# Kernel optimization log

Hardware: AMD Instinct MI355X
Metric: run time of the kernel (lower is better)

## Reference

```python
import jax, jax.numpy as jnp
import numpy as np

N = 50000   # nodes
E = 400000  # edges
H = 4       # heads
C = 64      # hidden per head
IN = 8
G = 64      # graphs in batch
NEG_SLOPE = 0.2


def setup_inputs() -> dict:
    key = jax.random.key(0)
    ks = jax.random.split(key, 32)
    def w(k, shape, fan_in):
        return jax.random.normal(k, shape, jnp.float32) * (1.0 / np.sqrt(fan_in))
    inp = {}
    inp['x'] = jax.random.normal(ks[0], (N, IN), jnp.float32)
    inp['edge_index'] = jax.random.randint(ks[1], (2, E), 0, N, jnp.int32)
    inp['edge_attr'] = jax.random.normal(ks[2], (E, 1), jnp.float32)
    inp['batch'] = jnp.sort(jax.random.randint(ks[3], (N,), 0, G, jnp.int32))
    # encoder
    inp['enc_w'] = w(ks[4], (IN, H * 16), IN)[:, :64]  # [8,64]
    inp['enc_b'] = jnp.zeros((64,), jnp.float32)
    # gat1: in 64 -> H*C = 256
    inp['g1_wl'] = w(ks[5], (64, H * C), 64)
    inp['g1_bl'] = jnp.zeros((H * C,), jnp.float32)
    inp['g1_wr'] = w(ks[6], (64, H * C), 64)
    inp['g1_we'] = w(ks[7], (1, H * C), 1)
    inp['g1_att'] = w(ks[8], (H, C), C)
    inp['g1_b'] = jnp.zeros((H * C,), jnp.float32)
    # gat2: in 256 -> H*C = 256
    inp['g2_wl'] = w(ks[9], (H * C, H * C), H * C)
    inp['g2_bl'] = jnp.zeros((H * C,), jnp.float32)
    inp['g2_wr'] = w(ks[10], (H * C, H * C), H * C)
    inp['g2_we'] = w(ks[11], (1, H * C), 1)
    inp['g2_att'] = w(ks[12], (H, C), C)
    inp['g2_b'] = jnp.zeros((H * C,), jnp.float32)
    # post MLP: 256 -> 128 -> LN -> ReLU -> 128 -> 64 -> ReLU
    inp['p1_w'] = w(ks[13], (H * C, 128), H * C)
    inp['p1_b'] = jnp.zeros((128,), jnp.float32)
    inp['ln_g'] = jnp.ones((128,), jnp.float32)
    inp['ln_b'] = jnp.zeros((128,), jnp.float32)
    inp['p2_w'] = w(ks[14], (128, 64), 128)
    inp['p2_b'] = jnp.zeros((64,), jnp.float32)
    inp['head_w'] = w(ks[15], (64, 1), 64)
    inp['head_b'] = jnp.zeros((1,), jnp.float32)
    return inp


def gatv2_conv(h, src, dst, ea, wl, bl, wr, we, att, b):
    # PyG GATv2Conv (concat=True): message from src j aggregated at dst i
    xl = (h @ wl + bl).reshape(N, H, C)   # lin_l(x_j), carries source messages
    xr = (h @ wr).reshape(N, H, C)        # lin_r(x_i)
    e = (ea @ we).reshape(E, H, C)        # lin_edge(edge_attr)
    s = jax.nn.leaky_relu(xl[src] + xr[dst] + e, NEG_SLOPE)  # [E,H,C]
    logits = jnp.einsum('ehc,hc->eh', s, att)                # [E,H]
    # softmax over incoming edges of each dst node
    mx = jax.ops.segment_max(logits, dst, num_segments=N)
    ex = jnp.exp(logits - mx[dst])
    denom = jax.ops.segment_sum(ex, dst, num_segments=N)
    alpha = ex / (denom[dst] + 1e-16)                        # [E,H]
    out = jax.ops.segment_sum(alpha[:, :, None] * xl[src], dst, num_segments=N)
    return out.reshape(N, H * C) + b


def reference(x, edge_index, edge_attr, batch, enc_w, enc_b,
              g1_wl, g1_bl, g1_wr, g1_we, g1_att, g1_b,
              g2_wl, g2_bl, g2_wr, g2_we, g2_att, g2_b,
              p1_w, p1_b, ln_g, ln_b, p2_w, p2_b, head_w, head_b):
    src, dst = edge_index[0], edge_index[1]
    h = jax.nn.relu(x @ enc_w + enc_b)
    h = jax.nn.relu(gatv2_conv(h, src, dst, edge_attr, g1_wl, g1_bl, g1_wr, g1_we, g1_att, g1_b))
    h = jax.nn.relu(gatv2_conv(h, src, dst, edge_attr, g2_wl, g2_bl, g2_wr, g2_we, g2_att, g2_b))
    # global mean pool per graph
    s = jax.ops.segment_sum(h, batch, num_segments=G)
    cnt = jax.ops.segment_sum(jnp.ones((N,), h.dtype), batch, num_segments=G)
    g = s / jnp.maximum(cnt, 1.0)[:, None]                   # [G, H*C]
    # post MLP (dropout is identity in eval)
    z = g @ p1_w + p1_b
    mu = jnp.mean(z, axis=-1, keepdims=True)
    var = jnp.mean((z - mu) ** 2, axis=-1, keepdims=True)
    z = (z - mu) * jax.lax.rsqrt(var + 1e-5) * ln_g + ln_b
    z = jax.nn.relu(z)
    z = jax.nn.relu(z @ p2_w + p2_b)
    return (z @ head_w + head_b).squeeze(-1)                 # [G]
```

## Files before the change

### kernel.cpp

```cpp
#include <hip/hip_runtime.h>
#include <hip/hip_bf16.h>
#include <math.h>

#define NN 50000
#define NE 400000
#define HH 4
#define CC 64
#define HC 256
#define GG 64
#define NB 196

typedef short v8s __attribute__((ext_vector_type(8)));
typedef float f32x4 __attribute__((ext_vector_type(4)));

static __device__ inline unsigned short f2bf(float v) {
  __hip_bfloat16 b = __float2bfloat16(v);
  return *reinterpret_cast<unsigned short*>(&b);
}
static __device__ inline float bflo(unsigned u) { return __uint_as_float(u << 16); }
static __device__ inline float bfhi(unsigned u) { return __uint_as_float(u & 0xffff0000u); }

__global__ __launch_bounds__(256) void encoder_kernel(
    const float* __restrict__ x, const float* __restrict__ w,
    const float* __restrict__ b, unsigned short* __restrict__ h0) {
  int idx = blockIdx.x * 256 + threadIdx.x;
  int node = idx >> 6, col = idx & 63;
  const float* xr = x + node * 8;
  float acc = b[col];
#pragma unroll
  for (int k = 0; k < 8; ++k) acc += xr[k] * w[k * 64 + col];
  h0[idx] = f2bf(fmaxf(acc, 0.f));
}

__global__ __launch_bounds__(256) void wconv_kernel(
    const float* __restrict__ W, int K, unsigned short* __restrict__ Wt) {
  int idx = blockIdx.x * 256 + threadIdx.x;
  if (idx >= K * 256) return;
  int k = idx >> 8, n = idx & 255;
  Wt[n * K + k] = f2bf(W[idx]);
}

template <int K, bool HAS_BIAS>
__global__ __launch_bounds__(256) void matmul_mfma_kernel(
    const unsigned short* __restrict__ A, const unsigned short* __restrict__ Wt,
    const float* __restrict__ bias, unsigned short* __restrict__ out, int M) {
  constexpr int AP = 40;
  __shared__ unsigned short a_lds[128 * AP];
  __shared__ unsigned short b_lds[128 * AP];
  const int tid = threadIdx.x;
  const int wave = tid >> 6;
  const int lane = tid & 63;
  const int quad = lane >> 4;
  const int lrow = lane & 15;
  const int wr = (wave & 1) * 64;
  const int wc = (wave >> 1) * 64;
  const int r0 = blockIdx.x * 128;
  const int n0 = blockIdx.y * 128;

  f32x4 acc[4][4];
#pragma unroll
  for (int i = 0; i < 4; ++i)
#pragma unroll
    for (int j = 0; j < 4; ++j) acc[i][j] = (f32x4){0.f, 0.f, 0.f, 0.f};

  const int srow = tid >> 1;
  const int shalf = tid & 1;
  int agrow = r0 + srow; if (agrow >= M) agrow = M - 1;
  const int bgrow = n0 + srow;

  for (int k0 = 0; k0 < K; k0 += 32) {
    {
      const float4* sa = (const float4*)&A[(size_t)agrow * K + k0 + shalf * 16];
      const float4* sb = (const float4*)&Wt[(size_t)bgrow * K + k0 + shalf * 16];
      float4 va0 = sa[0], va1 = sa[1];
      float4 vb0 = sb[0], vb1 = sb[1];
      *(float4*)&a_lds[srow * AP + shalf * 16]     = va0;
      *(float4*)&a_lds[srow * AP + shalf * 16 + 8] = va1;
      *(float4*)&b_lds[srow * AP + shalf * 16]     = vb0;
      *(float4*)&b_lds[srow * AP + shalf * 16 + 8] = vb1;
    }
    __syncthreads();

    v8s af[4], bf[4];
#pragma unroll
    for (int rt = 0; rt < 4; ++rt)
      af[rt] = *(const v8s*)&a_lds[(wr + rt * 16 + lrow) * AP + quad * 8];
#pragma unroll
    for (int ct = 0; ct < 4; ++ct)
      bf[ct] = *(const v8s*)&b_lds[(wc + ct * 16 + lrow) * AP + quad * 8];
#pragma unroll
    for (int rt = 0; rt < 4; ++rt)
#pragma unroll
      for (int ct = 0; ct < 4; ++ct)
        acc[rt][ct] = __builtin_amdgcn_mfma_f32_16x16x32_bf16(af[rt], bf[ct], acc[rt][ct], 0, 0, 0);
    __syncthreads();
  }

#pragma unroll
  for (int rt = 0; rt < 4; ++rt) {
    int mbase = r0 + wr + rt * 16 + quad * 4;
#pragma unroll
    for (int ct = 0; ct < 4; ++ct) {
      int col = n0 + wc + ct * 16 + lrow;
      float b = HAS_BIAS ? bias[col] : 0.f;
#pragma unroll
      for (int r = 0; r < 4; ++r) {
        int row = mbase + r;
        if (row < M) out[(size_t)row * 256 + col] = f2bf(acc[rt][ct][r] + b);
      }
    }
  }
}

__global__ void degree_kernel(const int* __restrict__ ei, int* __restrict__ deg) {
  int e = blockIdx.x * 256 + threadIdx.x;
  if (e < NE) atomicAdd(&deg[ei[NE + e]], 1);
}

__global__ __launch_bounds__(256) void blocksum_kernel(
    const int* __restrict__ deg, int* __restrict__ bsum) {
  int t = threadIdx.x;
  int i = blockIdx.x * 256 + t;
  int v = (i < NN) ? deg[i] : 0;
#pragma unroll
  for (int off = 32; off; off >>= 1) v += __shfl_down(v, off, 64);
  __shared__ int ws[4];
  if ((t & 63) == 0) ws[t >> 6] = v;
  __syncthreads();
  if (t == 0) bsum[blockIdx.x] = ws[0] + ws[1] + ws[2] + ws[3];
}

__global__ __launch_bounds__(256) void blockscan_kernel(
    const int* __restrict__ bsum, int* __restrict__ bpre, int* __restrict__ rowstart) {
  __shared__ int s[256];
  int t = threadIdx.x;
  int v = (t < NB) ? bsum[t] : 0;
  s[t] = v;
  __syncthreads();
  for (int off = 1; off < 256; off <<= 1) {
    int x = s[t];
    int y = (t >= off) ? s[t - off] : 0;
    __syncthreads();
    s[t] = x + y;
    __syncthreads();
  }
  if (t < NB) bpre[t] = s[t] - v;
  if (t == 255) rowstart[NN] = s[255];
}

__global__ __launch_bounds__(256) void rowstart_kernel(
    const int* __restrict__ deg, const int* __restrict__ bpre,
    int* __restrict__ rowstart, int* __restrict__ cursor) {
  __shared__ int s[256];
  int t = threadIdx.x;
  int i = blockIdx.x * 256 + t;
  int v = (i < NN) ? deg[i] : 0;
  s[t] = v;
  __syncthreads();
  for (int off = 1; off < 256; off <<= 1) {
    int x = s[t];
    int y = (t >= off) ? s[t - off] : 0;
    __syncthreads();
    s[t] = x + y;
    __syncthreads();
  }
  if (i < NN) {
    int rs = bpre[blockIdx.x] + s[t] - v;
    rowstart[i] = rs;
    cursor[i] = rs;
  }
}

__global__ void fill_kernel(const int* __restrict__ ei, const float* __restrict__ ea,
                            int* __restrict__ cursor, int2* __restrict__ edges) {
  int e = blockIdx.x * 256 + threadIdx.x;
  if (e < NE) {
    int d = ei[NE + e];
    int pos = atomicAdd(&cursor[d], 1);
    edges[pos] = make_int2(ei[e], __float_as_int(ea[e]));
  }
}

template <bool OUTBF>
__global__ __launch_bounds__(256) void gat_fused_kernel(
    const int* __restrict__ rowstart, const int2* __restrict__ edges,
    const unsigned short* __restrict__ xl, const unsigned short* __restrict__ xr,
    const float* __restrict__ we, const float* __restrict__ att,
    const float* __restrict__ bias, float* __restrict__ outf,
    unsigned short* __restrict__ outb) {
  int node = (blockIdx.x * 256 + threadIdx.x) >> 6;
  int lane = threadIdx.x & 63;
  int r0 = __builtin_amdgcn_readfirstlane(rowstart[node]);
  int r1 = __builtin_amdgcn_readfirstlane(rowstart[node + 1]);
  const uint2* xl2 = (const uint2*)xl;
  uint2 rp = ((const uint2*)xr)[(size_t)node * 64 + lane];
  float4 r = make_float4(bflo(rp.x), bfhi(rp.x), bflo(rp.y), bfhi(rp.y));
  float4 wv = ((const float4*)we)[lane];
  float4 at = ((const float4*)att)[lane];
  const float LOG2E = 1.442695040888963f;
  at.x *= LOG2E; at.y *= LOG2E; at.z *= LOG2E; at.w *= LOG2E;
  float4 acc = make_float4(0.f, 0.f, 0.f, 0.f);
  float denom = 0.f;

  auto edge_step = [&](float eav, uint2 p) {
    float4 a = make_float4(bflo(p.x), bfhi(p.x), bflo(p.y), bfhi(p.y));
    float s0 = a.x + (r.x + eav * wv.x);
    float s1 = a.y + (r.y + eav * wv.y);
    float s2 = a.z + (r.z + eav * wv.z);
    float s3 = a.w + (r.w + eav * wv.w);
    s0 = fmaxf(s0, 0.2f * s0);
    s1 = fmaxf(s1, 0.2f * s1);
    s2 = fmaxf(s2, 0.2f * s2);
    s3 = fmaxf(s3, 0.2f * s3);
    float p4 = (s0 * at.x + s1 * at.y) + (s2 * at.z + s3 * at.w);
#pragma unroll
    for (int off = 8; off; off >>= 1) p4 += __shfl_xor(p4, off, 16);
    float ex = exp2f(p4);
    denom += ex;
    acc.x += ex * a.x; acc.y += ex * a.y; acc.z += ex * a.z; acc.w += ex * a.w;
  };

  int i = r0;
  for (; i + 4 <= r1; i += 4) {
    int2 e0 = edges[i];
    int2 e1 = edges[i + 1];
    int2 e2 = edges[i + 2];
    int2 e3 = edges[i + 3];
    uint2 p0 = xl2[(size_t)e0.x * 64 + lane];
    uint2 p1 = xl2[(size_t)e1.x * 64 + lane];
    uint2 p2 = xl2[(size_t)e2.x * 64 + lane];
    uint2 p3 = xl2[(size_t)e3.x * 64 + lane];
    edge_step(__int_as_float(e0.y), p0);
    edge_step(__int_as_float(e1.y), p1);
    edge_step(__int_as_float(e2.y), p2);
    edge_step(__int_as_float(e3.y), p3);
  }
  for (; i < r1; ++i) {
    int2 e = edges[i];
    edge_step(__int_as_float(e.y), xl2[(size_t)e.x * 64 + lane]);
  }

  float inv = 1.f / (denom + 1e-16f);
  float4 bv = ((const float4*)bias)[lane];
  float4 o;
  o.x = fmaxf(acc.x * inv + bv.x, 0.f);
  o.y = fmaxf(acc.y * inv + bv.y, 0.f);
  o.z = fmaxf(acc.z * inv + bv.z, 0.f);
  o.w = fmaxf(acc.w * inv + bv.w, 0.f);
  if (OUTBF) {
    uint2 pk;
    pk.x = (unsigned)f2bf(o.x) | ((unsigned)f2bf(o.y) << 16);
    pk.y = (unsigned)f2bf(o.z) | ((unsigned)f2bf(o.w) << 16);
    ((uint2*)outb)[(size_t)node * 64 + lane] = pk;
  } else {
    ((float4*)outf)[(size_t)node * 64 + lane] = o;
  }
}

__global__ void seg_bounds_kernel(const int* __restrict__ batch, int* __restrict__ bounds) {
  int g = threadIdx.x;
  if (g > GG) return;
  int lo = 0, hi = NN;
  while (lo < hi) {
    int mid = (lo + hi) >> 1;
    if (batch[mid] < g) lo = mid + 1; else hi = mid;
  }
  bounds[g] = lo;
}

__global__ __launch_bounds__(256) void pool_kernel(
    const float* __restrict__ h, const int* __restrict__ batch,
    float* __restrict__ pool) {
  int rg = threadIdx.x >> 6;
  int lane = threadIdx.x & 63;
  int n0 = blockIdx.x * 64;
  const float4* h4 = (const float4*)h;
  float4 acc = make_float4(0.f, 0.f, 0.f, 0.f);
  int cur = -1;
#pragma unroll 4
  for (int i = 0; i < 16; ++i) {
    int n = n0 + rg + 4 * i;
    if (n >= NN) break;
    int b = batch[n];
    if (b != cur) {
      if (cur >= 0) {
        float* p = &pool[cur * 256 + lane * 4];
        atomicAdd(p + 0, acc.x); atomicAdd(p + 1, acc.y);
        atomicAdd(p + 2, acc.z); atomicAdd(p + 3, acc.w);
      }
      cur = b;
      acc = make_float4(0.f, 0.f, 0.f, 0.f);
    }
    float4 v = h4[(size_t)n * 64 + lane];
    acc.x += v.x; acc.y += v.y; acc.z += v.z; acc.w += v.w;
  }
  if (cur >= 0) {
    float* p = &pool[cur * 256 + lane * 4];
    atomicAdd(p + 0, acc.x); atomicAdd(p + 1, acc.y);
    atomicAdd(p + 2, acc.z); atomicAdd(p + 3, acc.w);
  }
}

__global__ __launch_bounds__(128) void mlp_kernel(
    const float* __restrict__ pool, const int* __restrict__ bounds,
    const float* __restrict__ p1w, const float* __restrict__ p1b,
    const float* __restrict__ lng, const float* __restrict__ lnb,
    const float* __restrict__ p2w, const float* __restrict__ p2b,
    const float* __restrict__ hw, const float* __restrict__ hb,
    float* __restrict__ out) {
  __shared__ float sg[256];
  __shared__ float red[128];
  __shared__ float sz[128];
  __shared__ float s2[64];
  int b = blockIdx.x, tid = threadIdx.x;
  float cntf = (float)(bounds[b + 1] - bounds[b]);
  float invc = 1.f / fmaxf(cntf, 1.f);
  for (int i = tid; i < 256; i += 128) sg[i] = pool[b * 256 + i] * invc;
  __syncthreads();
  float z = p1b[tid];
  for (int k = 0; k < 256; ++k) z += sg[k] * p1w[k * 128 + tid];
  red[tid] = z; __syncthreads();
  for (int off = 64; off; off >>= 1) { if (tid < off) red[tid] += red[tid + off]; __syncthreads(); }
  float mu = red[0] * (1.f / 128.f);
  __syncthreads();
  float d = z - mu;
  red[tid] = d * d; __syncthreads();
  for (int off = 64; off; off >>= 1) { if (tid < off) red[tid] += red[tid + off]; __syncthreads(); }
  float var = red[0] * (1.f / 128.f);
  float zn = d * rsqrtf(var + 1e-5f) * lng[tid] + lnb[tid];
  sz[tid] = fmaxf(zn, 0.f);
  __syncthreads();
  if (tid < 64) {
    float a = p2b[tid];
    for (int k = 0; k < 128; ++k) a += sz[k] * p2w[k * 64 + tid];
    s2[tid] = fmaxf(a, 0.f);
  }
  __syncthreads();
  if (tid < 64) {
    float p = s2[tid] * hw[tid];
    for (int off = 32; off; off >>= 1) p += __shfl_down(p, off, 64);
    if (tid == 0) out[b] = p + hb[0];
  }
}

extern "C" void kernel_launch(void* const* d_in, const int* in_sizes, int n_in,
                              void* d_out, int out_size, void* d_ws, size_t ws_size,
                              hipStream_t stream) {
  const float* x      = (const float*)d_in[0];
  const int*   ei     = (const int*)d_in[1];
  const float* ea     = (const float*)d_in[2];
  const int*   batch  = (const int*)d_in[3];
  const float* enc_w  = (const float*)d_in[4];
  const float* enc_b  = (const float*)d_in[5];
  const float* g1_wl  = (const float*)d_in[6];
  const float* g1_bl  = (const float*)d_in[7];
  const float* g1_wr  = (const float*)d_in[8];
  const float* g1_we  = (const float*)d_in[9];
  const float* g1_att = (const float*)d_in[10];
  const float* g1_b   = (const float*)d_in[11];
  const float* g2_wl  = (const float*)d_in[12];
  const float* g2_bl  = (const float*)d_in[13];
  const float* g2_wr  = (const float*)d_in[14];
  const float* g2_we  = (const float*)d_in[15];
  const float* g2_att = (const float*)d_in[16];
  const float* g2_b   = (const float*)d_in[17];
  const float* p1_w   = (const float*)d_in[18];
  const float* p1_b   = (const float*)d_in[19];
  const float* ln_g   = (const float*)d_in[20];
  const float* ln_b   = (const float*)d_in[21];
  const float* p2_w   = (const float*)d_in[22];
  const float* p2_b   = (const float*)d_in[23];
  const float* head_w = (const float*)d_in[24];
  const float* head_b = (const float*)d_in[25];
  float* out = (float*)d_out;

  char* ws = (char*)d_ws;
  size_t off = 0;
  auto alloc = [&](size_t bytes) -> void* {
    void* p = ws + off;
    off = (off + bytes + 255) & ~(size_t)255;
    return p;
  };
  unsigned short* xl   = (unsigned short*)alloc((size_t)NN * HC * 2);
  unsigned short* xr   = (unsigned short*)alloc((size_t)NN * HC * 2);
  float* hbuf      = (float*)alloc((size_t)NN * HC * 4);
  unsigned short* h0   = (unsigned short*)alloc((size_t)NN * 64 * 2);
  unsigned short* hb16 = (unsigned short*)alloc((size_t)NN * HC * 2);
  unsigned short* wt1l = (unsigned short*)alloc((size_t)64 * 256 * 2);
  unsigned short* wt1r = (unsigned short*)alloc((size_t)64 * 256 * 2);
  unsigned short* wt2l = (unsigned short*)alloc((size_t)256 * 256 * 2);
  unsigned short* wt2r = (unsigned short*)alloc((size_t)256 * 256 * 2);
  float* pool      = (float*)alloc((size_t)GG * HC * 4);
  int*   deg       = (int*)alloc((size_t)NN * 4);
  int*   rowstart  = (int*)alloc((size_t)(NN + 1) * 4);
  int*   cursor    = (int*)alloc((size_t)NN * 4);
  int*   bsum      = (int*)alloc((size_t)NB * 4);
  int*   bpre      = (int*)alloc((size_t)NB * 4);
  int2*  edges     = (int2*)alloc((size_t)NE * 8);
  int*   bounds    = (int*)alloc((size_t)(GG + 1) * 4);

  hipMemsetAsync(deg, 0, (size_t)NN * 4, stream);
  hipMemsetAsync(pool, 0, (size_t)GG * HC * 4, stream);

  encoder_kernel<<<NN * 64 / 256, 256, 0, stream>>>(x, enc_w, enc_b, h0);
  wconv_kernel<<<64, 256, 0, stream>>>(g1_wl, 64, wt1l);
  wconv_kernel<<<64, 256, 0, stream>>>(g1_wr, 64, wt1r);
  wconv_kernel<<<256, 256, 0, stream>>>(g2_wl, 256, wt2l);
  wconv_kernel<<<256, 256, 0, stream>>>(g2_wr, 256, wt2r);

  degree_kernel<<<(NE + 255) / 256, 256, 0, stream>>>(ei, deg);
  blocksum_kernel<<<NB, 256, 0, stream>>>(deg, bsum);
  blockscan_kernel<<<1, 256, 0, stream>>>(bsum, bpre, rowstart);
  rowstart_kernel<<<NB, 256, 0, stream>>>(deg, bpre, rowstart, cursor);
  fill_kernel<<<(NE + 255) / 256, 256, 0, stream>>>(ei, ea, cursor, edges);

  seg_bounds_kernel<<<1, GG + 1, 0, stream>>>(batch, bounds);

  dim3 mmg((NN + 127) / 128, 2);

  matmul_mfma_kernel<64, true><<<mmg, 256, 0, stream>>>(h0, wt1l, g1_bl, xl, NN);
  matmul_mfma_kernel<64, false><<<mmg, 256, 0, stream>>>(h0, wt1r, nullptr, xr, NN);
  gat_fused_kernel<true><<<NN / 4, 256, 0, stream>>>(rowstart, edges,
                                                     xl, xr, g1_we, g1_att, g1_b,
                                                     nullptr, hb16);

  matmul_mfma_kernel<256, true><<<mmg, 256, 0, stream>>>(hb16, wt2l, g2_bl, xl, NN);
  matmul_mfma_kernel<256, false><<<mmg, 256, 0, stream>>>(hb16, wt2r, nullptr, xr, NN);
  gat_fused_kernel<false><<<NN / 4, 256, 0, stream>>>(rowstart, edges,
                                                      xl, xr, g2_we, g2_att, g2_b,
                                                      hbuf, nullptr);

  pool_kernel<<<(NN + 63) / 64, 256, 0, stream>>>(hbuf, batch, pool);
  mlp_kernel<<<GG, 128, 0, stream>>>(pool, bounds, p1_w, p1_b, ln_g, ln_b,
                                     p2_w, p2_b, head_w, head_b, out);
}
```

Before: 371.9 us.

## Fuse left/right projections into one GEMM and fuse mean-pool into GAT kernel

Concatenates the lin_l and lin_r weights so that a single MFMA GEMM produces an interleaved [N,512] xl|xr buffer, removing one matmul launch per layer. The second GAT layer now reduces its outputs per block in shared memory and atomically adds them into the per-graph pool. This removes the fp32 hbuf write/read and the separate pool kernel. The edge gather loop is unrolled to 8 for more memory-level parallelism. The price is more float atomics and a wider gather stride, since each row is now 1 KB.

```diff
diff --git a/kernel.cpp b/kernel.cpp
--- a/kernel.cpp
+++ b/kernel.cpp
@@ -40,7 +40,7 @@
   Wt[n * K + k] = f2bf(W[idx]);
 }
 
-template <int K, bool HAS_BIAS>
+template <int K>
 __global__ __launch_bounds__(256) void matmul_mfma_kernel(
     const unsigned short* __restrict__ A, const unsigned short* __restrict__ Wt,
     const float* __restrict__ bias, unsigned short* __restrict__ out, int M) {
@@ -102,11 +102,11 @@
 #pragma unroll
     for (int ct = 0; ct < 4; ++ct) {
       int col = n0 + wc + ct * 16 + lrow;
-      float b = HAS_BIAS ? bias[col] : 0.f;
+      float b = (col < 256) ? bias[col] : 0.f;
 #pragma unroll
       for (int r = 0; r < 4; ++r) {
         int row = mbase + r;
-        if (row < M) out[(size_t)row * 256 + col] = f2bf(acc[rt][ct][r] + b);
+        if (row < M) out[(size_t)row * 512 + col] = f2bf(acc[rt][ct][r] + b);
       }
     }
   }
@@ -181,19 +181,20 @@
   }
 }
 
-template <bool OUTBF>
+template <bool POOL>
 __global__ __launch_bounds__(256) void gat_fused_kernel(
     const int* __restrict__ rowstart, const int2* __restrict__ edges,
-    const unsigned short* __restrict__ xl, const unsigned short* __restrict__ xr,
+    const unsigned short* __restrict__ xlr,
     const float* __restrict__ we, const float* __restrict__ att,
-    const float* __restrict__ bias, float* __restrict__ outf,
-    unsigned short* __restrict__ outb) {
-  int node = (blockIdx.x * 256 + threadIdx.x) >> 6;
+    const float* __restrict__ bias, const int* __restrict__ batch,
+    unsigned short* __restrict__ outb, float* __restrict__ pool) {
+  int wave = threadIdx.x >> 6;
+  int node = blockIdx.x * 4 + wave;
   int lane = threadIdx.x & 63;
   int r0 = __builtin_amdgcn_readfirstlane(rowstart[node]);
   int r1 = __builtin_amdgcn_readfirstlane(rowstart[node + 1]);
-  const uint2* xl2 = (const uint2*)xl;
-  uint2 rp = ((const uint2*)xr)[(size_t)node * 64 + lane];
+  const uint2* xlr2 = (const uint2*)xlr;
+  uint2 rp = xlr2[(size_t)node * 128 + 64 + lane];
   float4 r = make_float4(bflo(rp.x), bfhi(rp.x), bflo(rp.y), bfhi(rp.y));
   float4 wv = ((const float4*)we)[lane];
   float4 at = ((const float4*)att)[lane];
@@ -221,23 +222,43 @@
   };
 
   int i = r0;
-  for (; i + 4 <= r1; i += 4) {
-    int2 e0 = edges[i];
-    int2 e1 = edges[i + 1];
-    int2 e2 = edges[i + 2];
-    int2 e3 = edges[i + 3];
-    uint2 p0 = xl2[(size_t)e0.x * 64 + lane];
-    uint2 p1 = xl2[(size_t)e1.x * 64 + lane];
-    uint2 p2 = xl2[(size_t)e2.x * 64 + lane];
-    uint2 p3 = xl2[(size_t)e3.x * 64 + lane];
+  for (; i + 8 <= r1; i += 8) {
+    int2 e0 = edges[i];     int2 e1 = edges[i + 1];
+    int2 e2 = edges[i + 2]; int2 e3 = edges[i + 3];
+    int2 e4 = edges[i + 4]; int2 e5 = edges[i + 5];
+    int2 e6 = edges[i + 6]; int2 e7 = edges[i + 7];
+    uint2 p0 = xlr2[(size_t)e0.x * 128 + lane];
+    uint2 p1 = xlr2[(size_t)e1.x * 128 + lane];
+    uint2 p2 = xlr2[(size_t)e2.x * 128 + lane];
+    uint2 p3 = xlr2[(size_t)e3.x * 128 + lane];
+    uint2 p4 = xlr2[(size_t)e4.x * 128 + lane];
+    uint2 p5 = xlr2[(size_t)e5.x * 128 + lane];
+    uint2 p6 = xlr2[(size_t)e6.x * 128 + lane];
+    uint2 p7 = xlr2[(size_t)e7.x * 128 + lane];
     edge_step(__int_as_float(e0.y), p0);
     edge_step(__int_as_float(e1.y), p1);
     edge_step(__int_as_float(e2.y), p2);
     edge_step(__int_as_float(e3.y), p3);
+    edge_step(__int_as_float(e4.y), p4);
+    edge_step(__int_as_float(e5.y), p5);
+    edge_step(__int_as_float(e6.y), p6);
+    edge_step(__int_as_float(e7.y), p7);
+  }
+  for (; i + 4 <= r1; i += 4) {
+    int2 e0 = edges[i];     int2 e1 = edges[i + 1];
+    int2 e2 = edges[i + 2]; int2 e3 = edges[i + 3];
+    uint2 p0 = xlr2[(size_t)e0.x * 128 + lane];
+    uint2 p1 = xlr2[(size_t)e1.x * 128 + lane];
+    uint2 p2 = xlr2[(size_t)e2.x * 128 + lane];
+    uint2 p3 = xlr2[(size_t)e3.x * 128 + lane];
+    edge_step(__int_as_float(e0.y), p0);
+    edge_step(__int_as_float(e1.y), p1);
+    edge_step(__int_as_float(e2.y), p2);
+    edge_step(__int_as_float(e3.y), p3);
   }
   for (; i < r1; ++i) {
     int2 e = edges[i];
-    edge_step(__int_as_float(e.y), xl2[(size_t)e.x * 64 + lane]);
+    edge_step(__int_as_float(e.y), xlr2[(size_t)e.x * 128 + lane]);
   }
 
   float inv = 1.f / (denom + 1e-16f);
@@ -247,13 +268,34 @@
   o.y = fmaxf(acc.y * inv + bv.y, 0.f);
   o.z = fmaxf(acc.z * inv + bv.z, 0.f);
   o.w = fmaxf(acc.w * inv + bv.w, 0.f);
-  if (OUTBF) {
+
+  if (!POOL) {
     uint2 pk;
     pk.x = (unsigned)f2bf(o.x) | ((unsigned)f2bf(o.y) << 16);
     pk.y = (unsigned)f2bf(o.z) | ((unsigned)f2bf(o.w) << 16);
     ((uint2*)outb)[(size_t)node * 64 + lane] = pk;
   } else {
-    ((float4*)outf)[(size_t)node * 64 + lane] = o;
+    __shared__ float so[4][256];
+    __shared__ int sg[4];
+    *(float4*)&so[wave][lane * 4] = o;
+    if (lane == 0) sg[wave] = batch[node];
+    __syncthreads();
+    int tid = threadIdx.x;
+    if (tid < 256) {
+      float a = so[0][tid];
+      int cg = sg[0];
+#pragma unroll
+      for (int w = 1; w < 4; ++w) {
+        if (sg[w] == cg) {
+          a += so[w][tid];
+        } else {
+          atomicAdd(&pool[cg * 256 + tid], a);
+          cg = sg[w];
+          a = so[w][tid];
+        }
+      }
+      atomicAdd(&pool[cg * 256 + tid], a);
+    }
   }
 }
 
@@ -266,39 +308,6 @@
     if (batch[mid] < g) lo = mid + 1; else hi = mid;
   }
   bounds[g] = lo;
-}
-
-__global__ __launch_bounds__(256) void pool_kernel(
-    const float* __restrict__ h, const int* __restrict__ batch,
-    float* __restrict__ pool) {
-  int rg = threadIdx.x >> 6;
-  int lane = threadIdx.x & 63;
-  int n0 = blockIdx.x * 64;
-  const float4* h4 = (const float4*)h;
-  float4 acc = make_float4(0.f, 0.f, 0.f, 0.f);
-  int cur = -1;
-#pragma unroll 4
-  for (int i = 0; i < 16; ++i) {
-    int n = n0 + rg + 4 * i;
-    if (n >= NN) break;
-    int b = batch[n];
-    if (b != cur) {
-      if (cur >= 0) {
-        float* p = &pool[cur * 256 + lane * 4];
-        atomicAdd(p + 0, acc.x); atomicAdd(p + 1, acc.y);
-        atomicAdd(p + 2, acc.z); atomicAdd(p + 3, acc.w);
-      }
-      cur = b;
-      acc = make_float4(0.f, 0.f, 0.f, 0.f);
-    }
-    float4 v = h4[(size_t)n * 64 + lane];
-    acc.x += v.x; acc.y += v.y; acc.z += v.z; acc.w += v.w;
-  }
-  if (cur >= 0) {
-    float* p = &pool[cur * 256 + lane * 4];
-    atomicAdd(p + 0, acc.x); atomicAdd(p + 1, acc.y);
-    atomicAdd(p + 2, acc.z); atomicAdd(p + 3, acc.w);
-  }
 }
 
 __global__ __launch_bounds__(128) void mlp_kernel(
@@ -381,15 +390,11 @@
     off = (off + bytes + 255) & ~(size_t)255;
     return p;
   };
-  unsigned short* xl   = (unsigned short*)alloc((size_t)NN * HC * 2);
-  unsigned short* xr   = (unsigned short*)alloc((size_t)NN * HC * 2);
-  float* hbuf      = (float*)alloc((size_t)NN * HC * 4);
+  unsigned short* xlr  = (unsigned short*)alloc((size_t)NN * 512 * 2);
   unsigned short* h0   = (unsigned short*)alloc((size_t)NN * 64 * 2);
   unsigned short* hb16 = (unsigned short*)alloc((size_t)NN * HC * 2);
-  unsigned short* wt1l = (unsigned short*)alloc((size_t)64 * 256 * 2);
-  unsigned short* wt1r = (unsigned short*)alloc((size_t)64 * 256 * 2);
-  unsigned short* wt2l = (unsigned short*)alloc((size_t)256 * 256 * 2);
-  unsigned short* wt2r = (unsigned short*)alloc((size_t)256 * 256 * 2);
+  unsigned short* wt1  = (unsigned short*)alloc((size_t)512 * 64 * 2);
+  unsigned short* wt2  = (unsigned short*)alloc((size_t)512 * 256 * 2);
   float* pool      = (float*)alloc((size_t)GG * HC * 4);
   int*   deg       = (int*)alloc((size_t)NN * 4);
   int*   rowstart  = (int*)alloc((size_t)(NN + 1) * 4);
@@ -403,10 +408,10 @@
   hipMemsetAsync(pool, 0, (size_t)GG * HC * 4, stream);
 
   encoder_kernel<<<NN * 64 / 256, 256, 0, stream>>>(x, enc_w, enc_b, h0);
-  wconv_kernel<<<64, 256, 0, stream>>>(g1_wl, 64, wt1l);
-  wconv_kernel<<<64, 256, 0, stream>>>(g1_wr, 64, wt1r);
-  wconv_kernel<<<256, 256, 0, stream>>>(g2_wl, 256, wt2l);
-  wconv_kernel<<<256, 256, 0, stream>>>(g2_wr, 256, wt2r);
+  wconv_kernel<<<64, 256, 0, stream>>>(g1_wl, 64, wt1);
+  wconv_kernel<<<64, 256, 0, stream>>>(g1_wr, 64, wt1 + (size_t)256 * 64);
+  wconv_kernel<<<256, 256, 0, stream>>>(g2_wl, 256, wt2);
+  wconv_kernel<<<256, 256, 0, stream>>>(g2_wr, 256, wt2 + (size_t)256 * 256);
 
   degree_kernel<<<(NE + 255) / 256, 256, 0, stream>>>(ei, deg);
   blocksum_kernel<<<NB, 256, 0, stream>>>(deg, bsum);
@@ -416,21 +421,18 @@
 
   seg_bounds_kernel<<<1, GG + 1, 0, stream>>>(batch, bounds);
 
-  dim3 mmg((NN + 127) / 128, 2);
-
-  matmul_mfma_kernel<64, true><<<mmg, 256, 0, stream>>>(h0, wt1l, g1_bl, xl, NN);
-  matmul_mfma_kernel<64, false><<<mmg, 256, 0, stream>>>(h0, wt1r, nullptr, xr, NN);
-  gat_fused_kernel<true><<<NN / 4, 256, 0, stream>>>(rowstart, edges,
-                                                     xl, xr, g1_we, g1_att, g1_b,
-                                                     nullptr, hb16);
-
-  matmul_mfma_kernel<256, true><<<mmg, 256, 0, stream>>>(hb16, wt2l, g2_bl, xl, NN);
-  matmul_mfma_kernel<256, false><<<mmg, 256, 0, stream>>>(hb16, wt2r, nullptr, xr, NN);
-  gat_fused_kernel<false><<<NN / 4, 256, 0, stream>>>(rowstart, edges,
-                                                      xl, xr, g2_we, g2_att, g2_b,
-                                                      hbuf, nullptr);
-
-  pool_kernel<<<(NN + 63) / 64, 256, 0, stream>>>(hbuf, batch, pool);
+  dim3 mmg((NN + 127) / 128, 4);
+
+  matmul_mfma_kernel<64><<<mmg, 256, 0, stream>>>(h0, wt1, g1_bl, xlr, NN);
+  gat_fused_kernel<false><<<NN / 4, 256, 0, stream>>>(rowstart, edges, xlr,
+                                                      g1_we, g1_att, g1_b, batch,
+                                                      hb16, nullptr);
+
+  matmul_mfma_kernel<256><<<mmg, 256, 0, stream>>>(hb16, wt2, g2_bl, xlr, NN);
+  gat_fused_kernel<true><<<NN / 4, 256, 0, stream>>>(rowstart, edges, xlr,
+                                                     g2_we, g2_att, g2_b, batch,
+                                                     nullptr, pool);
+
   mlp_kernel<<<GG, 128, 0, stream>>>(pool, bounds, p1_w, p1_b, ln_g, ln_b,
                                      p2_w, p2_b, head_w, head_b, out);
 }
```

Result: slower. 393.5 us (+5.8%).
